# Optimization experiments

Hardware: AMD Instinct MI355X
Metric: run time of the kernel (lower is better)

Reference implementation:

```python
import jax, jax.numpy as jnp
import numpy as np

N = 2000        # num_genes (nodes)
E = 64000       # edges
Q = 200000      # query edges
F_IN = 512      # num_features
H = 64          # hidden
Q_PHASE = 0.25  # magnetic charge q
SIM_DIM = 64
LABELS = 2


def _msconv(xr, xi, src, dst, w, W, n):
    """MagNet/MSGNN Chebyshev conv, K=1, sym normalization, absolute degree.

    A_s = (A + A^T)/2, Theta_ij = 2*pi*q*(A_ij - A_ji),
    L_hat = L - I = -D^{-1/2} A_s D^{-1/2} * exp(i*Theta)  (lambda_max = 2)
    out = X @ W[0] + (L_hat X) @ W[1]   (real weights on complex signal)
    """
    # symmetrize: each directed edge contributes entries (src->dst) and (dst->src)
    ss = jnp.concatenate([src, dst])
    dd = jnp.concatenate([dst, src])
    ws = jnp.concatenate([w, w]) * 0.5
    theta = 2.0 * jnp.pi * Q_PHASE * jnp.concatenate([w, -w])
    # absolute degree of symmetrized adjacency
    deg = jax.ops.segment_sum(jnp.abs(ws), dd, num_segments=n)
    dinv = jnp.where(deg > 0, 1.0 / jnp.sqrt(deg), 0.0)
    norm = ws * dinv[ss] * dinv[dd]
    cr = -norm * jnp.cos(theta)  # real part of L_hat entries
    ci = -norm * jnp.sin(theta)  # imag part
    xrs, xis = xr[ss], xi[ss]
    t1r = jax.ops.segment_sum(cr[:, None] * xrs - ci[:, None] * xis, dd, num_segments=n)
    t1i = jax.ops.segment_sum(cr[:, None] * xis + ci[:, None] * xrs, dd, num_segments=n)
    return xr @ W[0] + t1r @ W[1], xi @ W[0] + t1i @ W[1]


def setup_inputs() -> dict:
    key = jax.random.key(0)
    ks = jax.random.split(key, 10)
    real = jax.random.normal(ks[0], (N, F_IN), jnp.float32)
    imag = jax.random.normal(ks[1], (N, F_IN), jnp.float32)
    edge_index = jax.random.randint(ks[2], (2, E), 0, N, dtype=jnp.int64)
    query_edges = jax.random.randint(ks[3], (Q, 2), 0, N, dtype=jnp.int64)
    all_embeddings = jax.random.normal(ks[4], (N * N, SIM_DIM), jnp.float32)
    edge_weight = jax.random.uniform(ks[5], (E,), jnp.float32)
    W1 = jax.random.normal(ks[6], (2, F_IN, H), jnp.float32) / np.sqrt(F_IN)
    W2 = jax.random.normal(ks[7], (2, H, H), jnp.float32) / np.sqrt(H)
    lin_w = jax.random.normal(ks[8], (4 * H + SIM_DIM, LABELS), jnp.float32) * 0.05
    lin_b = jnp.zeros((LABELS,), jnp.float32)
    return {"real": real, "imag": imag, "edge_index": edge_index,
            "query_edges": query_edges, "all_embeddings": all_embeddings,
            "edge_weight": edge_weight, "W1": W1, "W2": W2,
            "lin_w": lin_w, "lin_b": lin_b}


def reference(real, imag, edge_index, query_edges, all_embeddings, edge_weight,
              W1, W2, lin_w, lin_b):
    src, dst = edge_index[0], edge_index[1]
    for W in (W1, W2):
        real, imag = _msconv(real, imag, src, dst, edge_weight, W, N)
        mask = (real >= 0).astype(real.dtype)   # complex_relu
        real = real * mask
        imag = imag * mask
    ni, nj = query_edges[:, 0], query_edges[:, 1]
    sim = all_embeddings[ni * N + nj]           # vectorized per-edge lookup
    x = jnp.concatenate([real[ni], real[nj], imag[ni], imag[nj], sim], axis=-1)
    # eval mode: dropout is identity
    logits = x @ lin_w + lin_b
    return jax.nn.log_softmax(logits, axis=1)
```

## Files before the change

kernel.cpp:

```cpp
#include <hip/hip_runtime.h>
#include <math.h>

constexpr int N_NODES = 2000;
constexpr int F_IN    = 512;
constexpr int H       = 64;
constexpr int SLOT_SH = 8;

__device__ __forceinline__ void gemm_tile256(
    const float* __restrict__ A, const float* __restrict__ W,
    float (*As)[65], float (*Ws)[64],
    int r0, int K, float* __restrict__ C)
{
  int t  = threadIdx.x;
  int tx = t & 15, ty = t >> 4;
  float acc[4][4] = {};
  for (int k0 = 0; k0 < K; k0 += 64) {
    #pragma unroll
    for (int i = 0; i < 16; i++) {
      int idx = t + i * 256;
      int row = idx >> 6, kk = idx & 63;
      int gr = r0 + row;
      As[row][kk] = (gr < N_NODES) ? A[(size_t)gr * K + k0 + kk] : 0.f;
    }
    #pragma unroll
    for (int i = 0; i < 16; i++) {
      int idx = t + i * 256;
      int kk = idx >> 6, col = idx & 63;
      Ws[kk][col] = W[(size_t)(k0 + kk) * H + col];
    }
    __syncthreads();
    #pragma unroll
    for (int kk = 0; kk < 64; kk++) {
      float4 wv = *reinterpret_cast<const float4*>(&Ws[kk][tx * 4]);
      float av[4];
      #pragma unroll
      for (int r = 0; r < 4; r++) av[r] = As[ty * 4 + r][kk];
      #pragma unroll
      for (int r = 0; r < 4; r++) {
        acc[r][0] = fmaf(av[r], wv.x, acc[r][0]);
        acc[r][1] = fmaf(av[r], wv.y, acc[r][1]);
        acc[r][2] = fmaf(av[r], wv.z, acc[r][2]);
        acc[r][3] = fmaf(av[r], wv.w, acc[r][3]);
      }
    }
    __syncthreads();
  }
  #pragma unroll
  for (int r = 0; r < 4; r++) {
    int gr = r0 + ty * 4 + r;
    if (gr < N_NODES) {
      *reinterpret_cast<float4*>(&C[(size_t)gr * H + tx * 4]) =
          make_float4(acc[r][0], acc[r][1], acc[r][2], acc[r][3]);
    }
  }
}

__global__ __launch_bounds__(256) void fused1_kernel(
    const float* __restrict__ real, const float* __restrict__ imag,
    const float* __restrict__ W1,
    const int* __restrict__ ei, const float* __restrict__ ew,
    float* __restrict__ deg, int* __restrict__ cnt,
    int* __restrict__ nbr, float* __restrict__ cra, float* __restrict__ cia,
    float* __restrict__ P0r, float* __restrict__ P0i,
    float* __restrict__ P1r, float* __restrict__ P1i, int E)
{
  __shared__ float As[64][65];
  __shared__ float Ws[64][64];
  if (blockIdx.x < 128) {
    int bi = blockIdx.x;
    int which = bi & 3, tile = bi >> 2;
    const float* A = (which & 1) ? imag : real;
    const float* W = W1 + (size_t)(which >> 1) * F_IN * H;
    float* C = (which == 0) ? P0r : (which == 1) ? P0i
             : (which == 2) ? P1r : P1i;
    gemm_tile256(A, W, As, Ws, tile * 64, F_IN, C);
  } else {
    int e = (blockIdx.x - 128) * 256 + threadIdx.x;
    if (e < E) {
      int s = ei[e], d = ei[E + e];
      float ww = ew[e];
      float aw = fabsf(0.5f * ww);
      atomicAdd(&deg[d], aw);
      atomicAdd(&deg[s], aw);
      float sn, cs;
      sincosf(1.5707963267948966f * ww, &sn, &cs);
      float cr = -0.5f * ww * cs;
      float ci = -0.5f * ww * sn;
      int p1 = atomicAdd(&cnt[d], 1);
      int i1 = (d << SLOT_SH) + p1;
      nbr[i1] = s; cra[i1] = cr; cia[i1] = ci;
      int p2 = atomicAdd(&cnt[s], 1);
      int i2 = (s << SLOT_SH) + p2;
      nbr[i2] = d; cra[i2] = cr; cia[i2] = -ci;
    }
  }
}

__device__ __forceinline__ void agg_partial(
    const int* __restrict__ cnt, const int* __restrict__ nbr,
    const float* __restrict__ cra, const float* __restrict__ cia,
    const float* __restrict__ deg,
    const float* __restrict__ Pr, const float* __restrict__ Pi,
    int v, int h, int wv, float& aro, float& aio)
{
  int cv = cnt[v];
  float ar = 0.f, ai = 0.f;
  for (int j = wv; j < cv; j += 4) {
    int idx = (v << SLOT_SH) + j;
    int u = nbr[idx];
    float dg = deg[u];
    float du = (dg > 0.f) ? rsqrtf(dg) : 0.f;
    float cr = cra[idx] * du, ci = cia[idx] * du;
    float pr = Pr[u * H + h];
    float pi = Pi[u * H + h];
    ar = fmaf(cr, pr, ar); ar = fmaf(-ci, pi, ar);
    ai = fmaf(cr, pi, ai); ai = fmaf( ci, pr, ai);
  }
  aro = ar; aio = ai;
}

__global__ __launch_bounds__(256) void aggregate1_kernel(
    const int* __restrict__ cnt, const int* __restrict__ nbr,
    const float* __restrict__ cra, const float* __restrict__ cia,
    const float* __restrict__ deg,
    const float* __restrict__ P0r, const float* __restrict__ P0i,
    const float* __restrict__ P1r, const float* __restrict__ P1i,
    float* __restrict__ xr, float* __restrict__ xi)
{
  __shared__ float sr[4][64], si[4][64];
  int v = blockIdx.x;
  int h = threadIdx.x & 63;
  int wv = threadIdx.x >> 6;
  float ar, ai;
  agg_partial(cnt, nbr, cra, cia, deg, P1r, P1i, v, h, wv, ar, ai);
  sr[wv][h] = ar; si[wv][h] = ai;
  __syncthreads();
  if (wv == 0) {
    float dgv = deg[v];
    float dv = (dgv > 0.f) ? rsqrtf(dgv) : 0.f;
    ar = (sr[0][h] + sr[1][h] + sr[2][h] + sr[3][h]) * dv + P0r[v * H + h];
    ai = (si[0][h] + si[1][h] + si[2][h] + si[3][h]) * dv + P0i[v * H + h];
    if (ar < 0.f) { ar = 0.f; ai = 0.f; }
    xr[v * H + h] = ar;
    xi[v * H + h] = ai;
  }
}

__global__ __launch_bounds__(256) void gemm2_kernel(
    const float* __restrict__ xr, const float* __restrict__ xi,
    const float* __restrict__ W2,
    float* __restrict__ P0r, float* __restrict__ P0i,
    float* __restrict__ P1r, float* __restrict__ P1i)
{
  __shared__ float As[64][65];
  __shared__ float Ws[64][64];
  int bi = blockIdx.x;
  int which = bi & 3, tile = bi >> 2;
  const float* A = (which & 1) ? xi : xr;
  const float* W = W2 + (size_t)(which >> 1) * H * H;
  float* C = (which == 0) ? P0r : (which == 1) ? P0i
           : (which == 2) ? P1r : P1i;
  gemm_tile256(A, W, As, Ws, tile * 64, H, C);
}

__global__ __launch_bounds__(256) void aggregate2_kernel(
    const int* __restrict__ cnt, const int* __restrict__ nbr,
    const float* __restrict__ cra, const float* __restrict__ cia,
    const float* __restrict__ deg,
    const float* __restrict__ P0r, const float* __restrict__ P0i,
    const float* __restrict__ P1r, const float* __restrict__ P1i,
    const float* __restrict__ lw, const float* __restrict__ lb,
    float4* __restrict__ nuw)
{
  __shared__ float sr[4][64], si[4][64];
  int v = blockIdx.x;
  int h = threadIdx.x & 63;
  int wv = threadIdx.x >> 6;
  float ar, ai;
  agg_partial(cnt, nbr, cra, cia, deg, P1r, P1i, v, h, wv, ar, ai);
  sr[wv][h] = ar; si[wv][h] = ai;
  __syncthreads();
  if (wv == 0) {
    float dgv = deg[v];
    float dv = (dgv > 0.f) ? rsqrtf(dgv) : 0.f;
    ar = (sr[0][h] + sr[1][h] + sr[2][h] + sr[3][h]) * dv + P0r[v * H + h];
    ai = (si[0][h] + si[1][h] + si[2][h] + si[3][h]) * dv + P0i[v * H + h];
    if (ar < 0.f) { ar = 0.f; ai = 0.f; }
    const float2* lw2 = reinterpret_cast<const float2*>(lw);
    float2 l0 = lw2[h], l1 = lw2[64 + h], l2 = lw2[128 + h], l3 = lw2[192 + h];
    float u0 = ar * l0.x + ai * l2.x;
    float u1 = ar * l0.y + ai * l2.y;
    float w0 = ar * l1.x + ai * l3.x;
    float w1 = ar * l1.y + ai * l3.y;
    #pragma unroll
    for (int off = 1; off < 64; off <<= 1) {
      u0 += __shfl_xor(u0, off, 64);
      u1 += __shfl_xor(u1, off, 64);
      w0 += __shfl_xor(w0, off, 64);
      w1 += __shfl_xor(w1, off, 64);
    }
    if (h == 0)
      nuw[v] = make_float4(u0 + lb[0], u1 + lb[1], w0, w1);
  }
}

__global__ __launch_bounds__(256) void query_kernel(
    const int* __restrict__ qe, const float* __restrict__ emb,
    const float* __restrict__ lw, const float4* __restrict__ nuw,
    float2* __restrict__ out, int Qn, int n)
{
  const float2* lw2 = reinterpret_cast<const float2*>(lw);
  int l = threadIdx.x & 15;
  float2 wa = lw2[256 + 4 * l];
  float2 wb = lw2[257 + 4 * l];
  float2 wc = lw2[258 + 4 * l];
  float2 wd = lw2[259 + 4 * l];
  int g0 = (blockIdx.x * 256 + threadIdx.x) >> 4;
  int ng = (gridDim.x * 256) >> 4;
  const float4* emb4 = reinterpret_cast<const float4*>(emb);
  for (int q = g0; q < Qn; q += 2 * ng) {
    int q2 = q + ng;
    bool has2 = q2 < Qn;
    int ni0 = qe[2 * q], nj0 = qe[2 * q + 1];
    int ni1 = has2 ? qe[2 * q2] : ni0;
    int nj1 = has2 ? qe[2 * q2 + 1] : nj0;
    float4 sa = emb4[((size_t)ni0 * n + nj0) * 16 + l];
    float4 sb = emb4[((size_t)ni1 * n + nj1) * 16 + l];
    float a0 = sa.x * wa.x + sa.y * wb.x + sa.z * wc.x + sa.w * wd.x;
    float a1 = sa.x * wa.y + sa.y * wb.y + sa.z * wc.y + sa.w * wd.y;
    float b0 = sb.x * wa.x + sb.y * wb.x + sb.z * wc.x + sb.w * wd.x;
    float b1 = sb.x * wa.y + sb.y * wb.y + sb.z * wc.y + sb.w * wd.y;
    #pragma unroll
    for (int off = 1; off < 16; off <<= 1) {
      a0 += __shfl_xor(a0, off, 64);
      a1 += __shfl_xor(a1, off, 64);
      b0 += __shfl_xor(b0, off, 64);
      b1 += __shfl_xor(b1, off, 64);
    }
    if (l == 0) {
      float4 uni = nuw[ni0];
      float4 unj = nuw[nj0];
      float lg0 = a0 + uni.x + unj.z;
      float lg1 = a1 + uni.y + unj.w;
      float m = fmaxf(lg0, lg1);
      float lse = m + logf(expf(lg0 - m) + expf(lg1 - m));
      out[q] = make_float2(lg0 - lse, lg1 - lse);
      if (has2) {
        float4 uni2 = nuw[ni1];
        float4 unj2 = nuw[nj1];
        float mg0 = b0 + uni2.x + unj2.z;
        float mg1 = b1 + uni2.y + unj2.w;
        float m2 = fmaxf(mg0, mg1);
        float lse2 = m2 + logf(expf(mg0 - m2) + expf(mg1 - m2));
        out[q2] = make_float2(mg0 - lse2, mg1 - lse2);
      }
    }
  }
}

extern "C" void kernel_launch(void* const* d_in, const int* in_sizes, int n_in,
                              void* d_out, int out_size, void* d_ws, size_t ws_size,
                              hipStream_t stream)
{
  const float* real = (const float*)d_in[0];
  const float* imag = (const float*)d_in[1];
  const int*   ei   = (const int*)d_in[2];
  const int*   qe   = (const int*)d_in[3];
  const float* emb  = (const float*)d_in[4];
  const float* ew   = (const float*)d_in[5];
  const float* W1   = (const float*)d_in[6];
  const float* W2   = (const float*)d_in[7];
  const float* lw   = (const float*)d_in[8];
  const float* lb   = (const float*)d_in[9];
  float2* out = (float2*)d_out;

  int E = in_sizes[2] / 2;
  int Q = in_sizes[3] / 2;
  int n = N_NODES;
  int nslots = N_NODES << SLOT_SH;

  char* ws = (char*)d_ws;
  size_t off = 0;
  auto alloc = [&](size_t bytes) -> char* {
    char* p = ws + off;
    off = (off + bytes + 255) & ~(size_t)255;
    return p;
  };
  float*  deg = (float*)alloc(2048 * 4);
  int*    cnt = (int*)  alloc(2048 * 4);
  int*    nbr = (int*)  alloc((size_t)nslots * 4);
  float*  cra = (float*)alloc((size_t)nslots * 4);
  float*  cia = (float*)alloc((size_t)nslots * 4);
  float*  P0r = (float*)alloc((size_t)n * H * 4);
  float*  P0i = (float*)alloc((size_t)n * H * 4);
  float*  P1r = (float*)alloc((size_t)n * H * 4);
  float*  P1i = (float*)alloc((size_t)n * H * 4);
  float*  xr1 = (float*)alloc((size_t)n * H * 4);
  float*  xi1 = (float*)alloc((size_t)n * H * 4);
  float4* nuw = (float4*)alloc((size_t)n * 16);

  hipMemsetAsync(deg, 0, 2 * 2048 * 4, stream);

  int eblocks = (E + 255) / 256;
  fused1_kernel<<<128 + eblocks, 256, 0, stream>>>(
      real, imag, W1, ei, ew, deg, cnt, nbr, cra, cia,
      P0r, P0i, P1r, P1i, E);
  aggregate1_kernel<<<n, 256, 0, stream>>>(cnt, nbr, cra, cia, deg,
                                           P0r, P0i, P1r, P1i, xr1, xi1);
  gemm2_kernel<<<128, 256, 0, stream>>>(xr1, xi1, W2, P0r, P0i, P1r, P1i);
  aggregate2_kernel<<<n, 256, 0, stream>>>(cnt, nbr, cra, cia, deg,
                                           P0r, P0i, P1r, P1i, lw, lb, nuw);
  query_kernel<<<2048, 256, 0, stream>>>(qe, emb, lw, nuw, out, Q, n);
}
```

Measured before the change: 144.4 us.

## Overlap embedding gather with first-layer GEMM and edge build in one launch

Moves the heavy per-query similarity gather and dot-product into the first fused kernel so it runs alongside the edge CSR build and the first GEMM. The query path is split: partial similarity logits go to a workspace buffer, and a light head kernel later adds the node terms and applies log-softmax. The GEMM K-tile also shrinks from 64 to 32 to cut shared memory, which raises occupancy for the combined kernel. The costs are an extra Q-sized intermediate write and read, and GEMM blocks scheduled after the many query blocks may start late.

```diff
diff --git a/kernel.cpp b/kernel.cpp
--- a/kernel.cpp
+++ b/kernel.cpp
@@ -5,32 +5,33 @@
 constexpr int F_IN    = 512;
 constexpr int H       = 64;
 constexpr int SLOT_SH = 8;
+constexpr int GBLK    = 1664;
 
 __device__ __forceinline__ void gemm_tile256(
     const float* __restrict__ A, const float* __restrict__ W,
-    float (*As)[65], float (*Ws)[64],
+    float (*As)[33], float (*Ws)[64],
     int r0, int K, float* __restrict__ C)
 {
   int t  = threadIdx.x;
   int tx = t & 15, ty = t >> 4;
   float acc[4][4] = {};
-  for (int k0 = 0; k0 < K; k0 += 64) {
+  for (int k0 = 0; k0 < K; k0 += 32) {
     #pragma unroll
-    for (int i = 0; i < 16; i++) {
+    for (int i = 0; i < 8; i++) {
       int idx = t + i * 256;
-      int row = idx >> 6, kk = idx & 63;
+      int row = idx >> 5, kk = idx & 31;
       int gr = r0 + row;
       As[row][kk] = (gr < N_NODES) ? A[(size_t)gr * K + k0 + kk] : 0.f;
     }
     #pragma unroll
-    for (int i = 0; i < 16; i++) {
+    for (int i = 0; i < 8; i++) {
       int idx = t + i * 256;
       int kk = idx >> 6, col = idx & 63;
       Ws[kk][col] = W[(size_t)(k0 + kk) * H + col];
     }
     __syncthreads();
     #pragma unroll
-    for (int kk = 0; kk < 64; kk++) {
+    for (int kk = 0; kk < 32; kk++) {
       float4 wv = *reinterpret_cast<const float4*>(&Ws[kk][tx * 4]);
       float av[4];
       #pragma unroll
@@ -55,27 +56,57 @@
   }
 }
 
-__global__ __launch_bounds__(256) void fused1_kernel(
+__global__ __launch_bounds__(256) void mega_kernel(
     const float* __restrict__ real, const float* __restrict__ imag,
     const float* __restrict__ W1,
     const int* __restrict__ ei, const float* __restrict__ ew,
+    const int* __restrict__ qe, const float* __restrict__ emb,
+    const float* __restrict__ lw,
     float* __restrict__ deg, int* __restrict__ cnt,
     int* __restrict__ nbr, float* __restrict__ cra, float* __restrict__ cia,
     float* __restrict__ P0r, float* __restrict__ P0i,
-    float* __restrict__ P1r, float* __restrict__ P1i, int E)
-{
-  __shared__ float As[64][65];
-  __shared__ float Ws[64][64];
-  if (blockIdx.x < 128) {
-    int bi = blockIdx.x;
-    int which = bi & 3, tile = bi >> 2;
-    const float* A = (which & 1) ? imag : real;
-    const float* W = W1 + (size_t)(which >> 1) * F_IN * H;
-    float* C = (which == 0) ? P0r : (which == 1) ? P0i
-             : (which == 2) ? P1r : P1i;
-    gemm_tile256(A, W, As, Ws, tile * 64, F_IN, C);
-  } else {
-    int e = (blockIdx.x - 128) * 256 + threadIdx.x;
+    float* __restrict__ P1r, float* __restrict__ P1i,
+    float2* __restrict__ sl, int E, int Qn, int eblocks)
+{
+  __shared__ float As[64][33];
+  __shared__ float Ws[32][64];
+  int b = blockIdx.x;
+  if (b < GBLK) {
+    const float2* lw2 = reinterpret_cast<const float2*>(lw);
+    int l = threadIdx.x & 15;
+    float2 wa = lw2[256 + 4 * l];
+    float2 wb = lw2[257 + 4 * l];
+    float2 wc = lw2[258 + 4 * l];
+    float2 wd = lw2[259 + 4 * l];
+    int g0 = (b * 256 + threadIdx.x) >> 4;
+    int ng = (GBLK * 256) >> 4;
+    const float4* emb4 = reinterpret_cast<const float4*>(emb);
+    for (int q = g0; q < Qn; q += 2 * ng) {
+      int q2 = q + ng;
+      bool has2 = q2 < Qn;
+      int ni0 = qe[2 * q], nj0 = qe[2 * q + 1];
+      int ni1 = has2 ? qe[2 * q2] : ni0;
+      int nj1 = has2 ? qe[2 * q2 + 1] : nj0;
+      float4 sa = emb4[((size_t)ni0 * N_NODES + nj0) * 16 + l];
+      float4 sb = emb4[((size_t)ni1 * N_NODES + nj1) * 16 + l];
+      float a0 = sa.x * wa.x + sa.y * wb.x + sa.z * wc.x + sa.w * wd.x;
+      float a1 = sa.x * wa.y + sa.y * wb.y + sa.z * wc.y + sa.w * wd.y;
+      float b0 = sb.x * wa.x + sb.y * wb.x + sb.z * wc.x + sb.w * wd.x;
+      float b1 = sb.x * wa.y + sb.y * wb.y + sb.z * wc.y + sb.w * wd.y;
+      #pragma unroll
+      for (int off = 1; off < 16; off <<= 1) {
+        a0 += __shfl_xor(a0, off, 64);
+        a1 += __shfl_xor(a1, off, 64);
+        b0 += __shfl_xor(b0, off, 64);
+        b1 += __shfl_xor(b1, off, 64);
+      }
+      if (l == 0) {
+        sl[q] = make_float2(a0, a1);
+        if (has2) sl[q2] = make_float2(b0, b1);
+      }
+    }
+  } else if (b < GBLK + eblocks) {
+    int e = (b - GBLK) * 256 + threadIdx.x;
     if (e < E) {
       int s = ei[e], d = ei[E + e];
       float ww = ew[e];
@@ -93,6 +124,14 @@
       int i2 = (s << SLOT_SH) + p2;
       nbr[i2] = d; cra[i2] = cr; cia[i2] = -ci;
     }
+  } else {
+    int bi = b - GBLK - eblocks;
+    int which = bi & 3, tile = bi >> 2;
+    const float* A = (which & 1) ? imag : real;
+    const float* W = W1 + (size_t)(which >> 1) * F_IN * H;
+    float* C = (which == 0) ? P0r : (which == 1) ? P0i
+             : (which == 2) ? P1r : P1i;
+    gemm_tile256(A, W, As, Ws, tile * 64, F_IN, C);
   }
 }
 
@@ -152,8 +191,8 @@
     float* __restrict__ P0r, float* __restrict__ P0i,
     float* __restrict__ P1r, float* __restrict__ P1i)
 {
-  __shared__ float As[64][65];
-  __shared__ float Ws[64][64];
+  __shared__ float As[64][33];
+  __shared__ float Ws[32][64];
   int bi = blockIdx.x;
   int which = bi & 3, tile = bi >> 2;
   const float* A = (which & 1) ? xi : xr;
@@ -204,58 +243,21 @@
   }
 }
 
-__global__ __launch_bounds__(256) void query_kernel(
-    const int* __restrict__ qe, const float* __restrict__ emb,
-    const float* __restrict__ lw, const float4* __restrict__ nuw,
-    float2* __restrict__ out, int Qn, int n)
-{
-  const float2* lw2 = reinterpret_cast<const float2*>(lw);
-  int l = threadIdx.x & 15;
-  float2 wa = lw2[256 + 4 * l];
-  float2 wb = lw2[257 + 4 * l];
-  float2 wc = lw2[258 + 4 * l];
-  float2 wd = lw2[259 + 4 * l];
-  int g0 = (blockIdx.x * 256 + threadIdx.x) >> 4;
-  int ng = (gridDim.x * 256) >> 4;
-  const float4* emb4 = reinterpret_cast<const float4*>(emb);
-  for (int q = g0; q < Qn; q += 2 * ng) {
-    int q2 = q + ng;
-    bool has2 = q2 < Qn;
-    int ni0 = qe[2 * q], nj0 = qe[2 * q + 1];
-    int ni1 = has2 ? qe[2 * q2] : ni0;
-    int nj1 = has2 ? qe[2 * q2 + 1] : nj0;
-    float4 sa = emb4[((size_t)ni0 * n + nj0) * 16 + l];
-    float4 sb = emb4[((size_t)ni1 * n + nj1) * 16 + l];
-    float a0 = sa.x * wa.x + sa.y * wb.x + sa.z * wc.x + sa.w * wd.x;
-    float a1 = sa.x * wa.y + sa.y * wb.y + sa.z * wc.y + sa.w * wd.y;
-    float b0 = sb.x * wa.x + sb.y * wb.x + sb.z * wc.x + sb.w * wd.x;
-    float b1 = sb.x * wa.y + sb.y * wb.y + sb.z * wc.y + sb.w * wd.y;
-    #pragma unroll
-    for (int off = 1; off < 16; off <<= 1) {
-      a0 += __shfl_xor(a0, off, 64);
-      a1 += __shfl_xor(a1, off, 64);
-      b0 += __shfl_xor(b0, off, 64);
-      b1 += __shfl_xor(b1, off, 64);
-    }
-    if (l == 0) {
-      float4 uni = nuw[ni0];
-      float4 unj = nuw[nj0];
-      float lg0 = a0 + uni.x + unj.z;
-      float lg1 = a1 + uni.y + unj.w;
-      float m = fmaxf(lg0, lg1);
-      float lse = m + logf(expf(lg0 - m) + expf(lg1 - m));
-      out[q] = make_float2(lg0 - lse, lg1 - lse);
-      if (has2) {
-        float4 uni2 = nuw[ni1];
-        float4 unj2 = nuw[nj1];
-        float mg0 = b0 + uni2.x + unj2.z;
-        float mg1 = b1 + uni2.y + unj2.w;
-        float m2 = fmaxf(mg0, mg1);
-        float lse2 = m2 + logf(expf(mg0 - m2) + expf(mg1 - m2));
-        out[q2] = make_float2(mg0 - lse2, mg1 - lse2);
-      }
-    }
-  }
+__global__ __launch_bounds__(256) void head_kernel(
+    const int* __restrict__ qe, const float2* __restrict__ sl,
+    const float4* __restrict__ nuw, float2* __restrict__ out, int Qn)
+{
+  int q = blockIdx.x * 256 + threadIdx.x;
+  if (q >= Qn) return;
+  int2 nij = reinterpret_cast<const int2*>(qe)[q];
+  float2 s = sl[q];
+  float4 ui = nuw[nij.x];
+  float4 wj = nuw[nij.y];
+  float lg0 = s.x + ui.x + wj.z;
+  float lg1 = s.y + ui.y + wj.w;
+  float m = fmaxf(lg0, lg1);
+  float lse = m + logf(expf(lg0 - m) + expf(lg1 - m));
+  out[q] = make_float2(lg0 - lse, lg1 - lse);
 }
 
 extern "C" void kernel_launch(void* const* d_in, const int* in_sizes, int n_in,
@@ -298,17 +300,18 @@
   float*  xr1 = (float*)alloc((size_t)n * H * 4);
   float*  xi1 = (float*)alloc((size_t)n * H * 4);
   float4* nuw = (float4*)alloc((size_t)n * 16);
+  float2* sl  = (float2*)alloc((size_t)Q * 8);
 
   hipMemsetAsync(deg, 0, 2 * 2048 * 4, stream);
 
   int eblocks = (E + 255) / 256;
-  fused1_kernel<<<128 + eblocks, 256, 0, stream>>>(
-      real, imag, W1, ei, ew, deg, cnt, nbr, cra, cia,
-      P0r, P0i, P1r, P1i, E);
+  mega_kernel<<<GBLK + eblocks + 128, 256, 0, stream>>>(
+      real, imag, W1, ei, ew, qe, emb, lw,
+      deg, cnt, nbr, cra, cia, P0r, P0i, P1r, P1i, sl, E, Q, eblocks);
   aggregate1_kernel<<<n, 256, 0, stream>>>(cnt, nbr, cra, cia, deg,
                                            P0r, P0i, P1r, P1i, xr1, xi1);
   gemm2_kernel<<<128, 256, 0, stream>>>(xr1, xi1, W2, P0r, P0i, P1r, P1i);
   aggregate2_kernel<<<n, 256, 0, stream>>>(cnt, nbr, cra, cia, deg,
                                            P0r, P0i, P1r, P1i, lw, lb, nuw);
-  query_kernel<<<2048, 256, 0, stream>>>(qe, emb, lw, nuw, out, Q, n);
-}
+  head_kernel<<<(Q + 255) / 256, 256, 0, stream>>>(qe, sl, nuw, out, Q);
+}
```

Result: no change. 145.2 us (+0.5%).
